# Kernel tuning notes

Hardware: AMD Instinct MI355X
Metric: run time of the kernel (lower is better)

## Reference

```python
import math
import jax, jax.numpy as jnp
import numpy as np

N_HEAD = 8


def setup_inputs() -> dict:
    key = jax.random.key(0)
    ks = jax.random.split(key, 9)
    B, S, D = 4, 2048, 512
    s = 1.0 / math.sqrt(D)
    return {
        "x": jax.random.normal(ks[0], (B, S, D), jnp.float32),
        "Wq": jax.random.normal(ks[1], (D, D), jnp.float32) * s,
        "bq": jax.random.normal(ks[2], (D,), jnp.float32) * s,
        "Wk": jax.random.normal(ks[3], (D, D), jnp.float32) * s,
        "bk": jax.random.normal(ks[4], (D,), jnp.float32) * s,
        "Wv": jax.random.normal(ks[5], (D, D), jnp.float32) * s,
        "bv": jax.random.normal(ks[6], (D,), jnp.float32) * s,
        "Wo": jax.random.normal(ks[7], (D, D), jnp.float32) * s,
        "bo": jax.random.normal(ks[8], (D,), jnp.float32) * s,
    }


def reference(x, Wq, bq, Wk, bk, Wv, bv, Wo, bo):
    B, S, D = x.shape
    H = N_HEAD
    hd = D // H
    # projections -> [B, H, S, hd]
    def split_heads(y):
        return y.reshape(B, S, H, hd).transpose(0, 2, 1, 3)
    q = split_heads(x @ Wq + bq)
    k = split_heads(x @ Wk + bk)
    v = split_heads(x @ Wv + bv)
    scale = 1.0 / math.sqrt(hd)
    scores = jnp.einsum("bhqd,bhkd->bhqk", q, k) * scale  # [B,H,S,S]
    attn = jax.nn.softmax(scores, axis=-1)
    ctx = jnp.einsum("bhqk,bhkd->bhqd", attn, v)  # [B,H,S,hd]
    ctx = ctx.transpose(0, 2, 1, 3).reshape(B, S, D)
    out = ctx @ Wo + bo
    avg_attn = attn.mean(axis=1)  # [B,S,S]
    return out, avg_attn
```

## Files before the change

kernel.cpp:

```cpp
#include <hip/hip_runtime.h>

typedef __bf16 bf16;
typedef __bf16 bf16x8 __attribute__((ext_vector_type(8)));
typedef float  f32x4  __attribute__((ext_vector_type(4)));

#define MFMA16(a,b,c) __builtin_amdgcn_mfma_f32_16x16x32_bf16((a),(b),(c),0,0,0)

#define BATCH 4
#define SEQ   2048
#define DIM   512
#define NH    8
#define HD    64
#define QSCALE 0.18033688f

__device__ __forceinline__ bf16x8 ldsfrag(const bf16* t, int row, int kc, int quad){
    int unit = ((kc << 2) + quad) ^ (row & 7);
    return *(const bf16x8*)(t + row * 64 + unit * 8);
}

__device__ __forceinline__ void stage64x64(const bf16* src, long rowStride, bf16* dst, int tid){
#pragma unroll
    for (int rnd = 0; rnd < 2; ++rnd){
        int sid = tid + rnd * 256;
        int row = sid >> 3, s = sid & 7;
        bf16x8 val = *(const bf16x8*)(src + (long)row * rowStride + s * 8);
        *(bf16x8*)(dst + row * 64 + ((s ^ (row & 7)) << 3)) = val;
    }
}

__global__ __launch_bounds__(256) void cvt_x(const float* __restrict__ x, bf16* __restrict__ xb){
    int i = blockIdx.x * 256 + threadIdx.x;
    float4 f = ((const float4*)x)[i];
    bf16* o = xb + 4 * (long)i;
    o[0] = (bf16)f.x; o[1] = (bf16)f.y; o[2] = (bf16)f.z; o[3] = (bf16)f.w;
}

__global__ __launch_bounds__(256) void cvt_wt(const float* __restrict__ Wq, const float* __restrict__ Wk,
                                              const float* __restrict__ Wv, const float* __restrict__ Wo,
                                              bf16* __restrict__ WTb){
    int z = blockIdx.z;
    const float* W = (z == 0) ? Wq : (z == 1) ? Wk : (z == 2) ? Wv : Wo;
    bf16* WT = WTb + (long)z * DIM * DIM;
    __shared__ float lt[32 * 33];
    int t = threadIdx.x, r0 = t >> 5, c = t & 31;
    int k0 = blockIdx.x * 32, n0 = blockIdx.y * 32;
#pragma unroll
    for (int i = 0; i < 4; ++i){
        int row = r0 + i * 8;
        lt[row * 33 + c] = W[(long)(k0 + row) * DIM + n0 + c];
    }
    __syncthreads();
#pragma unroll
    for (int i = 0; i < 4; ++i){
        int nr = r0 + i * 8;
        WT[(long)(n0 + nr) * DIM + k0 + c] = (bf16)lt[c * 33 + nr];
    }
}

__global__ __launch_bounds__(256) void gemm_qkv(const bf16* __restrict__ X, const bf16* __restrict__ WTb,
                                                const float* __restrict__ bq, const float* __restrict__ bk,
                                                const float* __restrict__ bv, bf16* __restrict__ outb){
    __shared__ __align__(16) bf16 lA[128 * 64];
    __shared__ __align__(16) bf16 lB[128 * 64];
    int z = blockIdx.z;
    const bf16* WT = WTb + (long)z * DIM * DIM;
    const float* bias = (z == 0) ? bq : (z == 1) ? bk : bv;
    float qs = (z == 0) ? QSCALE : 1.0f;
    bf16* out = outb + (long)z * BATCH * SEQ * DIM;
    int tid = threadIdx.x, lane = tid & 63, w = tid >> 6;
    int wm = w >> 1, wn = w & 1;
    int m0 = blockIdx.y * 128, n0 = blockIdx.x * 128;
    int r16 = lane & 15, quad = lane >> 4;
    f32x4 zz = {0.f, 0.f, 0.f, 0.f};
    f32x4 acc[4][4];
#pragma unroll
    for (int a = 0; a < 4; ++a)
#pragma unroll
        for (int b2 = 0; b2 < 4; ++b2) acc[a][b2] = zz;

    for (int k0 = 0; k0 < DIM; k0 += 64){
        __syncthreads();
#pragma unroll
        for (int rnd = 0; rnd < 4; ++rnd){
            int sid = tid + rnd * 256;
            int row = sid >> 3, s = sid & 7;
            *(bf16x8*)(lA + row * 64 + ((s ^ (row & 7)) << 3)) =
                *(const bf16x8*)(X + (long)(m0 + row) * DIM + k0 + s * 8);
            *(bf16x8*)(lB + row * 64 + ((s ^ (row & 7)) << 3)) =
                *(const bf16x8*)(WT + (long)(n0 + row) * DIM + k0 + s * 8);
        }
        __syncthreads();
#pragma unroll
        for (int kc = 0; kc < 2; ++kc){
            bf16x8 aF[4], bF[4];
#pragma unroll
            for (int i = 0; i < 4; ++i){
                aF[i] = ldsfrag(lA, wm * 64 + i * 16 + r16, kc, quad);
                bF[i] = ldsfrag(lB, wn * 64 + i * 16 + r16, kc, quad);
            }
#pragma unroll
            for (int rb = 0; rb < 4; ++rb)
#pragma unroll
                for (int nb = 0; nb < 4; ++nb)
                    acc[rb][nb] = MFMA16(aF[rb], bF[nb], acc[rb][nb]);
        }
    }
#pragma unroll
    for (int nb = 0; nb < 4; ++nb){
        int col = n0 + wn * 64 + nb * 16 + r16;
        float bv_ = bias[col];
        int hh = col >> 6, d = col & 63;
#pragma unroll
        for (int rb = 0; rb < 4; ++rb)
#pragma unroll
            for (int r = 0; r < 4; ++r){
                int row = m0 + wm * 64 + rb * 16 + quad * 4 + r;
                int bb = row >> 11, s = row & 2047;
                out[((long)(bb * NH + hh) * SEQ + s) * HD + d] = (bf16)((acc[rb][nb][r] + bv_) * qs);
            }
    }
}

__global__ __launch_bounds__(256) void vtrans(const bf16* __restrict__ v, bf16* __restrict__ vT){
    __shared__ bf16 lt[64 * 72];
    int tid = threadIdx.x;
    int s0 = blockIdx.x * 64;
    int bh = blockIdx.z * NH + blockIdx.y;
#pragma unroll
    for (int rnd = 0; rnd < 2; ++rnd){
        int sid = tid + rnd * 256;
        int row = sid >> 3, sg = sid & 7;
        *(bf16x8*)(lt + row * 72 + sg * 8) =
            *(const bf16x8*)(v + ((long)bh * SEQ + s0 + row) * HD + sg * 8);
    }
    __syncthreads();
#pragma unroll
    for (int rnd = 0; rnd < 2; ++rnd){
        int sid = tid + rnd * 256;
        int d = sid >> 3, sg = sid & 7;
        bf16x8 o;
#pragma unroll
        for (int j = 0; j < 8; ++j) o[j] = lt[(sg * 8 + j) * 72 + d];
        *(bf16x8*)(vT + ((long)bh * HD + d) * SEQ + s0 + sg * 8) = o;
    }
}

__global__ __launch_bounds__(256) void attn_flash(const bf16* __restrict__ q, const bf16* __restrict__ k,
                                                  const bf16* __restrict__ vT, bf16* __restrict__ ctx,
                                                  float* __restrict__ llv_g){
    __shared__ __align__(16) bf16 lQ[64 * 64];
    __shared__ __align__(16) bf16 lK[64 * 64];
    __shared__ __align__(16) bf16 lV[64 * 64];
    __shared__ __align__(16) bf16 lP[4][16 * 64];
    int tid = threadIdx.x, lane = tid & 63, w = tid >> 6;
    int h = blockIdx.y, b = blockIdx.z;
    int bh = b * NH + h;
    int q0 = blockIdx.x * 64;
    int r16 = lane & 15, quad = lane >> 4;

    stage64x64(q + ((long)bh * SEQ + q0) * HD, HD, lQ, tid);
    __syncthreads();
    bf16x8 aF0 = ldsfrag(lQ, w * 16 + r16, 0, quad);
    bf16x8 aF1 = ldsfrag(lQ, w * 16 + r16, 1, quad);

    f32x4 zz = {0.f, 0.f, 0.f, 0.f};
    f32x4 ctxacc[4];
    float lsum[4] = {0.f, 0.f, 0.f, 0.f};
#pragma unroll
    for (int cb = 0; cb < 4; ++cb) ctxacc[cb] = zz;

    int r0_ = tid >> 3, s_ = tid & 7;
    const bf16* kbase = k + (long)bh * SEQ * HD;
    const bf16* vbase = vT + (long)bh * HD * SEQ;
    bf16x8 kr0, kr1, vr0, vr1;

    auto LOADREGS = [&](int j0){
        kr0 = *(const bf16x8*)(kbase + (long)(j0 + r0_) * HD + s_ * 8);
        kr1 = *(const bf16x8*)(kbase + (long)(j0 + r0_ + 32) * HD + s_ * 8);
        vr0 = *(const bf16x8*)(vbase + (long)r0_ * SEQ + j0 + s_ * 8);
        vr1 = *(const bf16x8*)(vbase + (long)(r0_ + 32) * SEQ + j0 + s_ * 8);
    };
    auto WRITELDS = [&](){
        int u = (s_ ^ (r0_ & 7)) << 3;
        *(bf16x8*)(lK + r0_ * 64 + u) = kr0;
        *(bf16x8*)(lK + (r0_ + 32) * 64 + u) = kr1;
        *(bf16x8*)(lV + r0_ * 64 + u) = vr0;
        *(bf16x8*)(lV + (r0_ + 32) * 64 + u) = vr1;
    };
    auto COMPUTE = [&](){
        __builtin_amdgcn_s_setprio(1);
#pragma unroll
        for (int cb = 0; cb < 4; ++cb){
            f32x4 sa = zz;
            sa = MFMA16(aF0, ldsfrag(lK, cb * 16 + r16, 0, quad), sa);
            sa = MFMA16(aF1, ldsfrag(lK, cb * 16 + r16, 1, quad), sa);
#pragma unroll
            for (int r = 0; r < 4; ++r){
                float p = __builtin_amdgcn_exp2f(sa[r]);
                lsum[r] += p;
                int row = quad * 4 + r, col = cb * 16 + r16;
                int unit = (col >> 3) ^ (row & 7);
                lP[w][row * 64 + unit * 8 + (col & 7)] = (bf16)p;
            }
        }
        asm volatile("s_waitcnt lgkmcnt(0)" ::: "memory");
        __builtin_amdgcn_sched_barrier(0);
#pragma unroll
        for (int kc = 0; kc < 2; ++kc){
            bf16x8 pF = ldsfrag(lP[w], r16, kc, quad);
#pragma unroll
            for (int cb = 0; cb < 4; ++cb)
                ctxacc[cb] = MFMA16(pF, ldsfrag(lV, cb * 16 + r16, kc, quad), ctxacc[cb]);
        }
        __builtin_amdgcn_s_setprio(0);
    };

    LOADREGS(0);
    WRITELDS();
    __syncthreads();
    for (int j0 = 0; j0 < SEQ - 64; j0 += 64){
        LOADREGS(j0 + 64);
        COMPUTE();
        __syncthreads();
        WRITELDS();
        __syncthreads();
    }
    COMPUTE();

#pragma unroll
    for (int m = 1; m < 16; m <<= 1)
#pragma unroll
        for (int r = 0; r < 4; ++r) lsum[r] += __shfl_xor(lsum[r], m, 64);
    float rinv[4];
#pragma unroll
    for (int r = 0; r < 4; ++r) rinv[r] = 1.0f / lsum[r];
#pragma unroll
    for (int cb = 0; cb < 4; ++cb)
#pragma unroll
        for (int r = 0; r < 4; ++r){
            long srow = q0 + w * 16 + quad * 4 + r;
            ctx[((long)b * SEQ + srow) * DIM + h * HD + cb * 16 + r16] = (bf16)(ctxacc[cb][r] * rinv[r]);
        }
    if (r16 == 0)
#pragma unroll
        for (int r = 0; r < 4; ++r)
            llv_g[(long)bh * SEQ + q0 + w * 16 + quad * 4 + r] = -__log2f(lsum[r]) - 3.0f;
}

__global__ __launch_bounds__(256) void attn_avg(const bf16* __restrict__ q, const bf16* __restrict__ k,
                                                const float* __restrict__ llv_g, float* __restrict__ avg){
    __shared__ __align__(16) bf16 lQ[64 * 64];
    __shared__ __align__(16) bf16 lK[64 * 64];
    __shared__ __align__(16) float lsOut[4][16 * 65];
    int lin  = blockIdx.x + (blockIdx.y << 5) + (blockIdx.z << 10);
    int task = ((lin & 7) << 9) + (lin >> 3);
    int qt = task & 31;
    int jt = (task >> 5) & 31;
    int b  = task >> 10;
    int tid = threadIdx.x, lane = tid & 63, w = tid >> 6;
    int r16 = lane & 15, quad = lane >> 4;
    int qbase = qt * 64;
    int j0 = jt * 64;

    f32x4 psum[4];
#pragma unroll
    for (int cb = 0; cb < 4; ++cb) psum[cb] = (f32x4){0.f, 0.f, 0.f, 0.f};

#pragma unroll 1
    for (int hh = 0; hh < NH; ++hh){
        long hA = (long)b * NH + hh;
        __syncthreads();
        stage64x64(q + (hA * SEQ + qbase) * HD, HD, lQ, tid);
        stage64x64(k + (hA * SEQ + j0) * HD, HD, lK, tid);
        f32x4 llv = *(const f32x4*)(llv_g + hA * SEQ + qbase + w * 16 + quad * 4);
        __syncthreads();
        bf16x8 aF0 = ldsfrag(lQ, w * 16 + r16, 0, quad);
        bf16x8 aF1 = ldsfrag(lQ, w * 16 + r16, 1, quad);
#pragma unroll
        for (int cb = 0; cb < 4; ++cb){
            f32x4 sa = MFMA16(aF0, ldsfrag(lK, cb * 16 + r16, 0, quad), llv);
            sa = MFMA16(aF1, ldsfrag(lK, cb * 16 + r16, 1, quad), sa);
#pragma unroll
            for (int r = 0; r < 4; ++r)
                psum[cb][r] += __builtin_amdgcn_exp2f(sa[r]);
        }
    }

#pragma unroll
    for (int cb = 0; cb < 4; ++cb)
#pragma unroll
        for (int r = 0; r < 4; ++r)
            lsOut[w][(quad * 4 + r) * 65 + cb * 16 + r16] = psum[cb][r];
#pragma unroll
    for (int i = 0; i < 4; ++i){
        int row  = ((i >> 1) << 3) + (lane >> 3);
        int col4 = ((i & 1) << 5) + ((lane & 7) << 2);
        f32x4 v = *(const f32x4*)(&lsOut[w][row * 65 + col4]);
        __builtin_nontemporal_store(v,
            (f32x4*)&avg[((long)b * SEQ + qbase + w * 16 + row) * SEQ + j0 + col4]);
    }
}

__global__ __launch_bounds__(256) void gemm_out(const bf16* __restrict__ CTX, const bf16* __restrict__ WT,
                                                const float* __restrict__ bo, float* __restrict__ out){
    __shared__ __align__(16) bf16 lA[128 * 64];
    __shared__ __align__(16) bf16 lB[128 * 64];
    int tid = threadIdx.x, lane = tid & 63, w = tid >> 6;
    int wm = w >> 1, wn = w & 1;
    int m0 = blockIdx.y * 128, n0 = blockIdx.x * 128;
    int r16 = lane & 15, quad = lane >> 4;
    f32x4 zz = {0.f, 0.f, 0.f, 0.f};
    f32x4 acc[4][4];
#pragma unroll
    for (int a = 0; a < 4; ++a)
#pragma unroll
        for (int b2 = 0; b2 < 4; ++b2) acc[a][b2] = zz;

    for (int k0 = 0; k0 < DIM; k0 += 64){
        __syncthreads();
#pragma unroll
        for (int rnd = 0; rnd < 4; ++rnd){
            int sid = tid + rnd * 256;
            int row = sid >> 3, s = sid & 7;
            *(bf16x8*)(lA + row * 64 + ((s ^ (row & 7)) << 3)) =
                *(const bf16x8*)(CTX + (long)(m0 + row) * DIM + k0 + s * 8);
            *(bf16x8*)(lB + row * 64 + ((s ^ (row & 7)) << 3)) =
                *(const bf16x8*)(WT + (long)(n0 + row) * DIM + k0 + s * 8);
        }
        __syncthreads();
#pragma unroll
        for (int kc = 0; kc < 2; ++kc){
            bf16x8 aF[4], bF[4];
#pragma unroll
            for (int i = 0; i < 4; ++i){
                aF[i] = ldsfrag(lA, wm * 64 + i * 16 + r16, kc, quad);
                bF[i] = ldsfrag(lB, wn * 64 + i * 16 + r16, kc, quad);
            }
#pragma unroll
            for (int rb2 = 0; rb2 < 4; ++rb2)
#pragma unroll
                for (int nb = 0; nb < 4; ++nb)
                    acc[rb2][nb] = MFMA16(aF[rb2], bF[nb], acc[rb2][nb]);
        }
    }
#pragma unroll
    for (int nb = 0; nb < 4; ++nb){
        int col = n0 + wn * 64 + nb * 16 + r16;
        float bv_ = bo[col];
#pragma unroll
        for (int rb2 = 0; rb2 < 4; ++rb2)
#pragma unroll
            for (int r = 0; r < 4; ++r){
                int row = m0 + wm * 64 + rb2 * 16 + quad * 4 + r;
                out[(long)row * DIM + col] = acc[rb2][nb][r] + bv_;
            }
    }
}

extern "C" void kernel_launch(void* const* d_in, const int* in_sizes, int n_in,
                              void* d_out, int out_size, void* d_ws, size_t ws_size,
                              hipStream_t stream) {
    const float* x  = (const float*)d_in[0];
    const float* Wq = (const float*)d_in[1];
    const float* bq = (const float*)d_in[2];
    const float* Wk = (const float*)d_in[3];
    const float* bk = (const float*)d_in[4];
    const float* Wv = (const float*)d_in[5];
    const float* bv = (const float*)d_in[6];
    const float* Wo = (const float*)d_in[7];
    const float* bo = (const float*)d_in[8];
    float* out = (float*)d_out;

    char* ws = (char*)d_ws;
    bf16*  xb   = (bf16*)(ws);
    bf16*  WT   = (bf16*)(ws + 8388608);
    bf16*  qb   = (bf16*)(ws + 10485760);
    bf16*  kb   = qb + (long)BATCH * SEQ * DIM;
    bf16*  vb   = kb + (long)BATCH * SEQ * DIM;
    bf16*  vT   = (bf16*)(ws + 35651584);
    bf16*  ctx  = (bf16*)(ws + 44040192);
    float* llv  = (float*)(ws + 52428800);

    cvt_x    <<<4096, 256, 0, stream>>>(x, xb);
    cvt_wt   <<<dim3(16, 16, 4), 256, 0, stream>>>(Wq, Wk, Wv, Wo, WT);
    gemm_qkv <<<dim3(4, 64, 3), 256, 0, stream>>>(xb, WT, bq, bk, bv, qb);
    vtrans   <<<dim3(32, 8, 4), 256, 0, stream>>>(vb, vT);
    attn_flash<<<dim3(32, 8, 4), 256, 0, stream>>>(qb, kb, vT, ctx, llv);
    attn_avg <<<dim3(32, 32, 4), 256, 0, stream>>>(qb, kb, llv, out + (long)BATCH * SEQ * DIM);
    gemm_out <<<dim3(4, 64), 256, 0, stream>>>(ctx, WT + 3L * DIM * DIM, bo, out);
}
```

Baseline: 251.2 us.

## Use 32x32 MFMA with 128-row Q tiles in flash attention; prefetch avg-kernel heads

The flash attention kernel now gives each wave 32 query rows using 32x32x16 bf16 MFMA, doubling the Q tile per block to 128 rows. This halves the number of K/V tile loads per query and gives each MFMA more work. The block index is remapped to interleave tasks across heads and batches. The attention-average kernel now prefetches the next head's Q/K into registers while computing the current head, overlapping global loads with math. In exchange, the flash grid shrinks to 512 blocks and uses more registers and LDS per block, which may lower occupancy.

```diff
diff --git a/kernel.cpp b/kernel.cpp
--- a/kernel.cpp
+++ b/kernel.cpp
@@ -3,8 +3,10 @@
 typedef __bf16 bf16;
 typedef __bf16 bf16x8 __attribute__((ext_vector_type(8)));
 typedef float  f32x4  __attribute__((ext_vector_type(4)));
+typedef float  f32x16 __attribute__((ext_vector_type(16)));
 
 #define MFMA16(a,b,c) __builtin_amdgcn_mfma_f32_16x16x32_bf16((a),(b),(c),0,0,0)
+#define MFMA32(a,b,c) __builtin_amdgcn_mfma_f32_32x32x16_bf16((a),(b),(c),0,0,0)
 
 #define BATCH 4
 #define SEQ   2048
@@ -16,6 +18,9 @@
 __device__ __forceinline__ bf16x8 ldsfrag(const bf16* t, int row, int kc, int quad){
     int unit = ((kc << 2) + quad) ^ (row & 7);
     return *(const bf16x8*)(t + row * 64 + unit * 8);
+}
+__device__ __forceinline__ bf16x8 ldsfrag32(const bf16* t, int row, int unit){
+    return *(const bf16x8*)(t + row * 64 + ((unit ^ (row & 7)) << 3));
 }
 
 __device__ __forceinline__ void stage64x64(const bf16* src, long rowStride, bf16* dst, int tid){
@@ -148,31 +153,44 @@
 __global__ __launch_bounds__(256) void attn_flash(const bf16* __restrict__ q, const bf16* __restrict__ k,
                                                   const bf16* __restrict__ vT, bf16* __restrict__ ctx,
                                                   float* __restrict__ llv_g){
-    __shared__ __align__(16) bf16 lQ[64 * 64];
+    __shared__ __align__(16) bf16 lQ[128 * 64];
     __shared__ __align__(16) bf16 lK[64 * 64];
     __shared__ __align__(16) bf16 lV[64 * 64];
-    __shared__ __align__(16) bf16 lP[4][16 * 64];
+    __shared__ __align__(16) bf16 lP[4][32 * 64];
     int tid = threadIdx.x, lane = tid & 63, w = tid >> 6;
-    int h = blockIdx.y, b = blockIdx.z;
+    int lin = blockIdx.x + (blockIdx.y << 4) + (blockIdx.z << 7);
+    int task = ((lin & 7) << 6) + (lin >> 3);
+    int qt = task & 15, h = (task >> 4) & 7, b = task >> 7;
     int bh = b * NH + h;
-    int q0 = blockIdx.x * 64;
-    int r16 = lane & 15, quad = lane >> 4;
-
-    stage64x64(q + ((long)bh * SEQ + q0) * HD, HD, lQ, tid);
+    int q0 = qt * 128;
+    int row32 = lane & 31, half = lane >> 5;
+    int r3 = row32 >> 3, c7 = row32 & 7;
+
+    {
+        const bf16* src = q + ((long)bh * SEQ + q0) * HD;
+#pragma unroll
+        for (int rnd = 0; rnd < 4; ++rnd){
+            int sid = tid + rnd * 256;
+            int row = sid >> 3, s = sid & 7;
+            *(bf16x8*)(lQ + row * 64 + ((s ^ (row & 7)) << 3)) =
+                *(const bf16x8*)(src + (long)row * HD + s * 8);
+        }
+    }
     __syncthreads();
-    bf16x8 aF0 = ldsfrag(lQ, w * 16 + r16, 0, quad);
-    bf16x8 aF1 = ldsfrag(lQ, w * 16 + r16, 1, quad);
-
-    f32x4 zz = {0.f, 0.f, 0.f, 0.f};
-    f32x4 ctxacc[4];
-    float lsum[4] = {0.f, 0.f, 0.f, 0.f};
-#pragma unroll
-    for (int cb = 0; cb < 4; ++cb) ctxacc[cb] = zz;
+    bf16x8 qF[4];
+#pragma unroll
+    for (int s = 0; s < 4; ++s) qF[s] = ldsfrag32(lQ, w * 32 + row32, 2 * s + half);
+
+    f32x16 ctxacc[2];
+    float lsum[16];
+#pragma unroll
+    for (int i = 0; i < 16; ++i){ ctxacc[0][i] = 0.f; ctxacc[1][i] = 0.f; lsum[i] = 0.f; }
 
     int r0_ = tid >> 3, s_ = tid & 7;
     const bf16* kbase = k + (long)bh * SEQ * HD;
     const bf16* vbase = vT + (long)bh * HD * SEQ;
     bf16x8 kr0, kr1, vr0, vr1;
+    bf16* lPw = lP[w];
 
     auto LOADREGS = [&](int j0){
         kr0 = *(const bf16x8*)(kbase + (long)(j0 + r0_) * HD + s_ * 8);
@@ -190,28 +208,32 @@
     auto COMPUTE = [&](){
         __builtin_amdgcn_s_setprio(1);
 #pragma unroll
-        for (int cb = 0; cb < 4; ++cb){
-            f32x4 sa = zz;
-            sa = MFMA16(aF0, ldsfrag(lK, cb * 16 + r16, 0, quad), sa);
-            sa = MFMA16(aF1, ldsfrag(lK, cb * 16 + r16, 1, quad), sa);
-#pragma unroll
-            for (int r = 0; r < 4; ++r){
-                float p = __builtin_amdgcn_exp2f(sa[r]);
-                lsum[r] += p;
-                int row = quad * 4 + r, col = cb * 16 + r16;
-                int unit = (col >> 3) ^ (row & 7);
-                lP[w][row * 64 + unit * 8 + (col & 7)] = (bf16)p;
+        for (int kb = 0; kb < 2; ++kb){
+            f32x16 sacc;
+#pragma unroll
+            for (int i = 0; i < 16; ++i) sacc[i] = 0.f;
+#pragma unroll
+            for (int s = 0; s < 4; ++s)
+                sacc = MFMA32(qF[s], ldsfrag32(lK, kb * 32 + row32, 2 * s + half), sacc);
+#pragma unroll
+            for (int reg = 0; reg < 16; ++reg){
+                float pp = __builtin_amdgcn_exp2f(sacc[reg]);
+                lsum[reg] += pp;
+                int qr = (reg & 3) + 8 * (reg >> 2) + 4 * half;
+                int pu = ((kb ^ half) << 2) | (r3 ^ (reg & 3));
+                lPw[qr * 64 + pu * 8 + c7] = (bf16)pp;
             }
         }
         asm volatile("s_waitcnt lgkmcnt(0)" ::: "memory");
         __builtin_amdgcn_sched_barrier(0);
-#pragma unroll
-        for (int kc = 0; kc < 2; ++kc){
-            bf16x8 pF = ldsfrag(lP[w], r16, kc, quad);
-#pragma unroll
-            for (int cb = 0; cb < 4; ++cb)
-                ctxacc[cb] = MFMA16(pF, ldsfrag(lV, cb * 16 + r16, kc, quad), ctxacc[cb]);
-        }
+        bf16x8 pF[4];
+#pragma unroll
+        for (int ks = 0; ks < 4; ++ks) pF[ks] = ldsfrag32(lPw, row32, 2 * ks + half);
+#pragma unroll
+        for (int db = 0; db < 2; ++db)
+#pragma unroll
+            for (int ks = 0; ks < 4; ++ks)
+                ctxacc[db] = MFMA32(pF[ks], ldsfrag32(lV, db * 32 + row32, 2 * ks + half), ctxacc[db]);
         __builtin_amdgcn_s_setprio(0);
     };
 
@@ -228,23 +250,27 @@
     COMPUTE();
 
 #pragma unroll
-    for (int m = 1; m < 16; m <<= 1)
-#pragma unroll
-        for (int r = 0; r < 4; ++r) lsum[r] += __shfl_xor(lsum[r], m, 64);
-    float rinv[4];
-#pragma unroll
-    for (int r = 0; r < 4; ++r) rinv[r] = 1.0f / lsum[r];
-#pragma unroll
-    for (int cb = 0; cb < 4; ++cb)
-#pragma unroll
-        for (int r = 0; r < 4; ++r){
-            long srow = q0 + w * 16 + quad * 4 + r;
-            ctx[((long)b * SEQ + srow) * DIM + h * HD + cb * 16 + r16] = (bf16)(ctxacc[cb][r] * rinv[r]);
-        }
-    if (r16 == 0)
-#pragma unroll
-        for (int r = 0; r < 4; ++r)
-            llv_g[(long)bh * SEQ + q0 + w * 16 + quad * 4 + r] = -__log2f(lsum[r]) - 3.0f;
+    for (int m = 1; m < 32; m <<= 1)
+#pragma unroll
+        for (int reg = 0; reg < 16; ++reg) lsum[reg] += __shfl_xor(lsum[reg], m, 64);
+    float rinv[16];
+#pragma unroll
+    for (int reg = 0; reg < 16; ++reg) rinv[reg] = 1.0f / lsum[reg];
+#pragma unroll
+    for (int db = 0; db < 2; ++db)
+#pragma unroll
+        for (int reg = 0; reg < 16; ++reg){
+            int qr = (reg & 3) + 8 * (reg >> 2) + 4 * half;
+            long srow = q0 + w * 32 + qr;
+            ctx[((long)b * SEQ + srow) * DIM + h * HD + db * 32 + row32] =
+                (bf16)(ctxacc[db][reg] * rinv[reg]);
+        }
+    if (row32 == 0)
+#pragma unroll
+        for (int reg = 0; reg < 16; ++reg){
+            int qr = (reg & 3) + 8 * (reg >> 2) + 4 * half;
+            llv_g[(long)bh * SEQ + q0 + w * 32 + qr] = -__log2f(lsum[reg]) - 3.0f;
+        }
 }
 
 __global__ __launch_bounds__(256) void attn_avg(const bf16* __restrict__ q, const bf16* __restrict__ k,
@@ -262,18 +288,36 @@
     int qbase = qt * 64;
     int j0 = jt * 64;
 
+    int r0_ = tid >> 3, s_ = tid & 7;
+    int u_ = (s_ ^ (r0_ & 7)) << 3;
+    bf16x8 qr0, qr1, kr0, kr1;
+    auto LOADA = [&](int hh){
+        long hA = (long)b * NH + hh;
+        const bf16* qh = q + (hA * SEQ + qbase) * HD;
+        const bf16* kh = k + (hA * SEQ + j0) * HD;
+        qr0 = *(const bf16x8*)(qh + (long)r0_ * HD + s_ * 8);
+        qr1 = *(const bf16x8*)(qh + (long)(r0_ + 32) * HD + s_ * 8);
+        kr0 = *(const bf16x8*)(kh + (long)r0_ * HD + s_ * 8);
+        kr1 = *(const bf16x8*)(kh + (long)(r0_ + 32) * HD + s_ * 8);
+    };
+    auto WRITEA = [&](){
+        *(bf16x8*)(lQ + r0_ * 64 + u_) = qr0;
+        *(bf16x8*)(lQ + (r0_ + 32) * 64 + u_) = qr1;
+        *(bf16x8*)(lK + r0_ * 64 + u_) = kr0;
+        *(bf16x8*)(lK + (r0_ + 32) * 64 + u_) = kr1;
+    };
+
     f32x4 psum[4];
 #pragma unroll
     for (int cb = 0; cb < 4; ++cb) psum[cb] = (f32x4){0.f, 0.f, 0.f, 0.f};
 
+    LOADA(0);
+    WRITEA();
+    __syncthreads();
 #pragma unroll 1
     for (int hh = 0; hh < NH; ++hh){
-        long hA = (long)b * NH + hh;
-        __syncthreads();
-        stage64x64(q + (hA * SEQ + qbase) * HD, HD, lQ, tid);
-        stage64x64(k + (hA * SEQ + j0) * HD, HD, lK, tid);
-        f32x4 llv = *(const f32x4*)(llv_g + hA * SEQ + qbase + w * 16 + quad * 4);
-        __syncthreads();
+        if (hh < NH - 1) LOADA(hh + 1);
+        f32x4 llv = *(const f32x4*)(llv_g + ((long)b * NH + hh) * SEQ + qbase + w * 16 + quad * 4);
         bf16x8 aF0 = ldsfrag(lQ, w * 16 + r16, 0, quad);
         bf16x8 aF1 = ldsfrag(lQ, w * 16 + r16, 1, quad);
 #pragma unroll
@@ -283,6 +327,11 @@
 #pragma unroll
             for (int r = 0; r < 4; ++r)
                 psum[cb][r] += __builtin_amdgcn_exp2f(sa[r]);
+        }
+        __syncthreads();
+        if (hh < NH - 1){
+            WRITEA();
+            __syncthreads();
         }
     }
 
@@ -385,7 +434,7 @@
     cvt_wt   <<<dim3(16, 16, 4), 256, 0, stream>>>(Wq, Wk, Wv, Wo, WT);
     gemm_qkv <<<dim3(4, 64, 3), 256, 0, stream>>>(xb, WT, bq, bk, bv, qb);
     vtrans   <<<dim3(32, 8, 4), 256, 0, stream>>>(vb, vT);
-    attn_flash<<<dim3(32, 8, 4), 256, 0, stream>>>(qb, kb, vT, ctx, llv);
+    attn_flash<<<dim3(16, 8, 4), 256, 0, stream>>>(qb, kb, vT, ctx, llv);
     attn_avg <<<dim3(32, 32, 4), 256, 0, stream>>>(qb, kb, llv, out + (long)BATCH * SEQ * DIM);
     gemm_out <<<dim3(4, 64), 256, 0, stream>>>(ctx, WT + 3L * DIM * DIM, bo, out);
 }
```

Result: faster. 246.0 us (-2.1%).
